# Kernel optimization log

Hardware: AMD Instinct MI355X
Metric: run time of the kernel (lower is better)

Reference implementation:

```python
import jax, jax.numpy as jnp
import numpy as np

D_MODEL = 1024
N_HEADS = 16
D_K = D_MODEL // N_HEADS
SCALE = float(np.sqrt(D_K))


def setup_inputs() -> dict:
    key = jax.random.key(0)
    ks = jax.random.split(key, 11)
    B, L, D = 2, 2048, D_MODEL
    s = 1.0 / np.sqrt(D)
    inp = {
        "q": jax.random.normal(ks[0], (B, L, D), dtype=jnp.float32),
        "k": jax.random.normal(ks[1], (B, L, D), dtype=jnp.float32),
        "v": jax.random.normal(ks[2], (B, L, D), dtype=jnp.float32),
        "Wq": jax.random.normal(ks[3], (D, D), dtype=jnp.float32) * s,
        "bq": jnp.zeros((D,), dtype=jnp.float32),
        "Wk": jax.random.normal(ks[4], (D, D), dtype=jnp.float32) * s,
        "bk": jnp.zeros((D,), dtype=jnp.float32),
        "Wv": jax.random.normal(ks[5], (D, D), dtype=jnp.float32) * s,
        "bv": jnp.zeros((D,), dtype=jnp.float32),
        "Wo": jax.random.normal(ks[6], (D, D), dtype=jnp.float32) * s,
        "bo": jnp.zeros((D,), dtype=jnp.float32),
    }
    return inp


def reference(q, k, v, Wq, bq, Wk, bk, Wv, bv, Wo, bo):
    B, L, D = q.shape
    H, Dk = N_HEADS, D_K
    # projections: [B,L,D] -> [B,H,L,Dk]
    def proj(x, W, b):
        y = x @ W + b
        return y.reshape(B, -1, H, Dk).transpose(0, 2, 1, 3)
    qh = proj(q, Wq, bq)
    kh = proj(k, Wk, bk)
    vh = proj(v, Wv, bv)
    # scores [B,H,Lq,Lk]
    scores = jnp.einsum("bhqd,bhkd->bhqk", qh, kh) / SCALE
    attn = jax.nn.softmax(scores, axis=-1)  # dropout=0.0 -> identity
    out = jnp.einsum("bhqk,bhkd->bhqd", attn, vh)
    out = out.transpose(0, 2, 1, 3).reshape(B, -1, D)
    return out @ Wo + bo
```

## Files before the change

kernel.cpp:

```cpp
#include <hip/hip_runtime.h>
#include <hip/hip_bf16.h>
#include <stdint.h>
#include <stddef.h>

typedef unsigned short ushortT;
typedef __attribute__((ext_vector_type(8))) short bf16x8s;
typedef __attribute__((ext_vector_type(4))) float f32x4;


__device__ __forceinline__ short f2bf(float f) {
  unsigned u = __float_as_uint(f);
  u += 0x7FFFu + ((u >> 16) & 1u);
  return (short)(u >> 16);
}

__device__ __forceinline__ unsigned pk_bf16(float a, float b) {
  __hip_bfloat162 h = __float22bfloat162_rn(make_float2(a, b));
  return *(unsigned*)&h;
}

__device__ __forceinline__ bf16x8s cvt8(const float* src) {
  const float4* p = (const float4*)src;
  float4 a = p[0], b = p[1];
  bf16x8s r;
  r[0] = f2bf(a.x); r[1] = f2bf(a.y); r[2] = f2bf(a.z); r[3] = f2bf(a.w);
  r[4] = f2bf(b.x); r[5] = f2bf(b.y); r[6] = f2bf(b.z); r[7] = f2bf(b.w);
  return r;
}

__device__ __forceinline__ void load_lds16(const ushortT* g, ushortT* l) {
  __builtin_amdgcn_global_load_lds(
      (const __attribute__((address_space(1))) void*)(g),
      (__attribute__((address_space(3))) void*)(l), 16, 0, 0);
}

__global__ __launch_bounds__(256)
void prep(const float* __restrict__ q, const float* __restrict__ k,
          const float* __restrict__ v,
          const float* __restrict__ Wq, const float* __restrict__ Wk,
          const float* __restrict__ Wv, const float* __restrict__ Wo,
          ushortT* __restrict__ Qc, ushortT* __restrict__ Kc,
          ushortT* __restrict__ Vc, ushortT* __restrict__ Wt)
{
  const int z = blockIdx.z;
  if (z < 4) {
    if (blockIdx.x >= 1024) return;
    __shared__ __align__(16) ushortT t[32][33];
    const float* W = (z == 0) ? Wq : (z == 1) ? Wk : (z == 2) ? Wv : Wo;
    ushortT* dst = Wt + (size_t)z * 1024 * 1024;
    const int x = (blockIdx.x & 31) * 32, y = (blockIdx.x >> 5) * 32;
    const int tx = threadIdx.x & 31, ty = threadIdx.x >> 5;
#pragma unroll
    for (int i = ty; i < 32; i += 8)
      t[i][tx] = (ushortT)f2bf(W[(size_t)(y + i) * 1024 + x + tx]);
    __syncthreads();
#pragma unroll
    for (int i = ty; i < 32; i += 8)
      dst[(size_t)(x + i) * 1024 + y + tx] = t[tx][i];
  } else {
    const float* src = (z == 4) ? q : (z == 5) ? k : v;
    ushortT* dst = (z == 4) ? Qc : (z == 5) ? Kc : Vc;
    const size_t i8 = ((size_t)blockIdx.x * 256 + threadIdx.x) * 8;
    *(bf16x8s*)(dst + i8) = cvt8(src + i8);
  }
}

__device__ __forceinline__ void gemm_core_128(
    const ushortT* __restrict__ A, const ushortT* __restrict__ Bt,
    int K, ushortT* As, ushortT* Bs, f32x4 (&acc)[4][4], int m0, int n0)
{
  const int tid  = threadIdx.x;
  const int wave = tid >> 6, lane = tid & 63;
  const int wm = (wave & 1) << 6;
  const int wn = (wave >> 1) << 6;
  const int lr = lane & 15;
  const int lk = (lane >> 4) << 3;

#pragma unroll
  for (int mi = 0; mi < 4; ++mi)
#pragma unroll
    for (int ni = 0; ni < 4; ++ni)
      acc[mi][ni] = (f32x4){0.f, 0.f, 0.f, 0.f};

  for (int k0 = 0; k0 < K; k0 += 32) {
    __syncthreads();
#pragma unroll
    for (int i = 0; i < 2; ++i) {
      const int cc  = tid + (i << 8);
      const int row = cc >> 2;
      const int ko  = (cc & 3) << 3;
      load_lds16(A  + (size_t)(m0 + row) * K + k0 + ko, As + cc * 8);
      load_lds16(Bt + (size_t)(n0 + row) * K + k0 + ko, Bs + cc * 8);
    }
    __syncthreads();

    bf16x8s af[4], bfr[4];
#pragma unroll
    for (int i = 0; i < 4; ++i)
      af[i] = *(const bf16x8s*)(As + (wm + i * 16 + lr) * 32 + lk);
#pragma unroll
    for (int i = 0; i < 4; ++i)
      bfr[i] = *(const bf16x8s*)(Bs + (wn + i * 16 + lr) * 32 + lk);

#pragma unroll
    for (int mi = 0; mi < 4; ++mi)
#pragma unroll
      for (int ni = 0; ni < 4; ++ni)
        acc[mi][ni] = __builtin_amdgcn_mfma_f32_16x16x32_bf16(
            af[mi], bfr[ni], acc[mi][ni], 0, 0, 0);
  }
}

__global__ __launch_bounds__(256)
void proj_gemm(const ushortT* __restrict__ Qc, const ushortT* __restrict__ Kc,
               const ushortT* __restrict__ Vc, const ushortT* __restrict__ WtAll,
               const float* __restrict__ bq, const float* __restrict__ bk,
               const float* __restrict__ bv,
               ushortT* __restrict__ Qh, ushortT* __restrict__ Kh,
               ushortT* __restrict__ Vt)
{
  __shared__ __align__(16) ushortT As[128 * 32];
  __shared__ __align__(16) ushortT Bs[128 * 32];
  const int which = blockIdx.z;
  const ushortT* A  = (which == 0) ? Qc : (which == 1) ? Kc : Vc;
  const ushortT* Bt = WtAll + (size_t)which * 1024 * 1024;
  const float* bias = (which == 0) ? bq : (which == 1) ? bk : bv;
  const int m0 = blockIdx.x * 128, n0 = blockIdx.y * 128;

  f32x4 acc[4][4];
  gemm_core_128(A, Bt, 1024, As, Bs, acc, m0, n0);

  const int lane = threadIdx.x & 63, wave = threadIdx.x >> 6;
  const int wm = (wave & 1) << 6, wn = (wave >> 1) << 6;
  const int lr = lane & 15, quad = lane >> 4;
  const float QSCALE = 0.18033688011112042f;

#pragma unroll
  for (int ni = 0; ni < 4; ++ni) {
    const int n = n0 + wn + ni * 16 + lr;
    const float bias_v = bias[n];
    const int h = n >> 6, d = n & 63;
#pragma unroll
    for (int mi = 0; mi < 4; ++mi) {
#pragma unroll
      for (int r = 0; r < 4; ++r) {
        const int m = m0 + wm + mi * 16 + quad * 4 + r;
        const int b = m >> 11, l = m & 2047;
        float val = acc[mi][ni][r] + bias_v;
        if (which == 0) val *= QSCALE;
        const ushortT o = (ushortT)f2bf(val);
        const size_t bh = (size_t)(b * 16 + h);
        if (which == 0)      Qh[(bh * 2048 + l) * 64 + d] = o;
        else if (which == 1) Kh[(bh * 2048 + l) * 64 + d] = o;
        else                 Vt[(bh * 64 + d) * 2048 + l] = o;
      }
    }
  }
}

__global__ __launch_bounds__(256)
void attn_kernel(const ushortT* __restrict__ Qh, const ushortT* __restrict__ Kh,
                 const ushortT* __restrict__ Vt, ushortT* __restrict__ Ob)
{
  const int b = blockIdx.z, h = blockIdx.y, qt = blockIdx.x;
  const int bh = b * 16 + h;
  const int wave = threadIdx.x >> 6, lane = threadIdx.x & 63;
  const int lr = lane & 15, quad = lane >> 4, lk = quad * 8;
  const int q0 = qt * 64 + wave * 16;

  const ushortT* Q = Qh + ((size_t)bh * 2048 + q0) * 64;
  const ushortT* K = Kh + (size_t)bh * 2048 * 64;
  const ushortT* V = Vt + (size_t)bh * 64 * 2048;

  __shared__ __align__(16) ushortT Ks[64 * 76];
  __shared__ __align__(16) ushortT Vs[64 * 76];
  __shared__ __align__(16) ushortT P4[4][16 * 88];
  ushortT* Pw = P4[wave];

  const bf16x8s qf0 = *(const bf16x8s*)(Q + lr * 64 + lk);
  const bf16x8s qf1 = *(const bf16x8s*)(Q + lr * 64 + 32 + lk);

  f32x4 o[4];
#pragma unroll
  for (int nt = 0; nt < 4; ++nt) o[nt] = (f32x4){0.f, 0.f, 0.f, 0.f};
  float lsum = 0.f;

  const int tid = threadIdx.x;
  const int srow = tid >> 3;
  const int sc8  = (tid & 7) << 3;

  for (int kt = 0; kt < 2048; kt += 64) {
    bf16x8s kch[2], vch[2];
#pragma unroll
    for (int i = 0; i < 2; ++i) {
      const int row = srow + i * 32;
      kch[i] = *(const bf16x8s*)(K + (size_t)(kt + row) * 64 + sc8);
      vch[i] = *(const bf16x8s*)(V + (size_t)row * 2048 + kt + sc8);
    }
    __syncthreads();
#pragma unroll
    for (int i = 0; i < 2; ++i) {
      const int row = srow + i * 32;
      *(bf16x8s*)(Ks + row * 76 + sc8) = kch[i];
      *(bf16x8s*)(Vs + row * 76 + sc8) = vch[i];
    }
    __syncthreads();

    f32x4 s[4];
#pragma unroll
    for (int t = 0; t < 4; ++t) s[t] = (f32x4){0.f, 0.f, 0.f, 0.f};
#pragma unroll
    for (int t = 0; t < 4; ++t) {
      const bf16x8s kf0 = *(const bf16x8s*)(Ks + (t * 16 + lr) * 76 + lk);
      const bf16x8s kf1 = *(const bf16x8s*)(Ks + (t * 16 + lr) * 76 + 32 + lk);
      s[t] = __builtin_amdgcn_mfma_f32_16x16x32_bf16(kf0, qf0, s[t], 0, 0, 0);
      s[t] = __builtin_amdgcn_mfma_f32_16x16x32_bf16(kf1, qf1, s[t], 0, 0, 0);
    }

#pragma unroll
    for (int t = 0; t < 4; ++t) {
      const float e0 = __builtin_amdgcn_exp2f(s[t][0]);
      const float e1 = __builtin_amdgcn_exp2f(s[t][1]);
      const float e2 = __builtin_amdgcn_exp2f(s[t][2]);
      const float e3 = __builtin_amdgcn_exp2f(s[t][3]);
      lsum += (e0 + e1) + (e2 + e3);
      uint2 d;
      d.x = pk_bf16(e0, e1);
      d.y = pk_bf16(e2, e3);
      *(uint2*)(Pw + lr * 88 + t * 16 + quad * 4) = d;
    }
    asm volatile("s_waitcnt lgkmcnt(0)" ::: "memory");

    const bf16x8s pf0 = *(const bf16x8s*)(Pw + lr * 88 + lk);
    const bf16x8s pf1 = *(const bf16x8s*)(Pw + lr * 88 + 32 + lk);
#pragma unroll
    for (int nt = 0; nt < 4; ++nt) {
      const bf16x8s vf0 = *(const bf16x8s*)(Vs + (nt * 16 + lr) * 76 + lk);
      const bf16x8s vf1 = *(const bf16x8s*)(Vs + (nt * 16 + lr) * 76 + 32 + lk);
      o[nt] = __builtin_amdgcn_mfma_f32_16x16x32_bf16(pf0, vf0, o[nt], 0, 0, 0);
      o[nt] = __builtin_amdgcn_mfma_f32_16x16x32_bf16(pf1, vf1, o[nt], 0, 0, 0);
    }
  }

  float* fP = (float*)Pw;
  {
    float s = lsum;
    s += __shfl_xor(s, 16);
    s += __shfl_xor(s, 32);
    fP[lr] = 1.0f / s;
  }
  asm volatile("s_waitcnt lgkmcnt(0)" ::: "memory");
  float invr[4];
#pragma unroll
  for (int r = 0; r < 4; ++r) invr[r] = fP[quad * 4 + r];

#pragma unroll
  for (int nt = 0; nt < 4; ++nt) {
    const int dcol = h * 64 + nt * 16 + lr;
#pragma unroll
    for (int r = 0; r < 4; ++r) {
      const int l = q0 + quad * 4 + r;
      Ob[((size_t)b * 2048 + l) * 1024 + dcol] = (ushortT)f2bf(o[nt][r] * invr[r]);
    }
  }
}

__global__ __launch_bounds__(256)
void out_gemm(const ushortT* __restrict__ Ob, const ushortT* __restrict__ Wto,
              const float* __restrict__ bo, float* __restrict__ C)
{
  __shared__ __align__(16) ushortT As[128 * 32];
  __shared__ __align__(16) ushortT Bs[128 * 32];
  const int m0 = blockIdx.x * 128, n0 = blockIdx.y * 128;

  f32x4 acc[4][4];
  gemm_core_128(Ob, Wto, 1024, As, Bs, acc, m0, n0);

  const int lane = threadIdx.x & 63, wave = threadIdx.x >> 6;
  const int wm = (wave & 1) << 6, wn = (wave >> 1) << 6;
  const int lr = lane & 15, quad = lane >> 4;

#pragma unroll
  for (int ni = 0; ni < 4; ++ni) {
    const int n = n0 + wn + ni * 16 + lr;
    const float bias_v = bo[n];
#pragma unroll
    for (int mi = 0; mi < 4; ++mi) {
#pragma unroll
      for (int r = 0; r < 4; ++r) {
        const int m = m0 + wm + mi * 16 + quad * 4 + r;
        C[(size_t)m * 1024 + n] = acc[mi][ni][r] + bias_v;
      }
    }
  }
}

extern "C" void kernel_launch(void* const* d_in, const int* in_sizes, int n_in,
                              void* d_out, int out_size, void* d_ws, size_t ws_size,
                              hipStream_t stream) {
  const float* q  = (const float*)d_in[0];
  const float* k  = (const float*)d_in[1];
  const float* v  = (const float*)d_in[2];
  const float* Wq = (const float*)d_in[3];
  const float* bq = (const float*)d_in[4];
  const float* Wk = (const float*)d_in[5];
  const float* bk = (const float*)d_in[6];
  const float* Wv = (const float*)d_in[7];
  const float* bv = (const float*)d_in[8];
  const float* Wo = (const float*)d_in[9];
  const float* bo = (const float*)d_in[10];

  char* ws = (char*)d_ws;
  ushortT* Wt = (ushortT*)(ws);
  ushortT* Qh = (ushortT*)(ws + (size_t)(8  << 20));
  ushortT* Kh = (ushortT*)(ws + (size_t)(16 << 20));
  ushortT* Vt = (ushortT*)(ws + (size_t)(24 << 20));
  ushortT* Qc = (ushortT*)(ws + (size_t)(32 << 20));
  ushortT* Kc = (ushortT*)(ws + (size_t)(40 << 20));
  ushortT* Vc = (ushortT*)(ws + (size_t)(48 << 20));
  ushortT* Ob = Qc;

  prep<<<dim3(2048, 1, 7), 256, 0, stream>>>(q, k, v, Wq, Wk, Wv, Wo,
                                             Qc, Kc, Vc, Wt);
  proj_gemm<<<dim3(32, 8, 3), 256, 0, stream>>>(Qc, Kc, Vc, Wt, bq, bk, bv,
                                                Qh, Kh, Vt);
  attn_kernel<<<dim3(32, 16, 2), 256, 0, stream>>>(Qh, Kh, Vt, Ob);
  out_gemm<<<dim3(32, 8), 256, 0, stream>>>(Ob, Wt + (size_t)3 * 1024 * 1024,
                                            bo, (float*)d_out);
}
```

Before: 243.2 us.

## Vectorize weight transpose, deepen GEMM K-step to 64, narrow out_gemm tiles

The weight transpose in prep now does float4 loads and ushort4 stores through a padded LDS tile instead of scalar accesses. The shared GEMM core moves from a K step of 32 to 64, which halves the number of barrier pairs per tile at the cost of twice the LDS. out_gemm switches to 128x64 tiles, doubling the grid to 512 blocks so more CUs have work. The 64-wide LDS rows with a 128-byte stride may cause bank conflicts on the fragment reads.

```diff
diff --git a/kernel.cpp b/kernel.cpp
--- a/kernel.cpp
+++ b/kernel.cpp
@@ -45,18 +45,27 @@
   const int z = blockIdx.z;
   if (z < 4) {
     if (blockIdx.x >= 1024) return;
-    __shared__ __align__(16) ushortT t[32][33];
+    __shared__ __align__(16) ushortT t[32][36];
     const float* W = (z == 0) ? Wq : (z == 1) ? Wk : (z == 2) ? Wv : Wo;
     ushortT* dst = Wt + (size_t)z * 1024 * 1024;
     const int x = (blockIdx.x & 31) * 32, y = (blockIdx.x >> 5) * 32;
-    const int tx = threadIdx.x & 31, ty = threadIdx.x >> 5;
-#pragma unroll
-    for (int i = ty; i < 32; i += 8)
-      t[i][tx] = (ushortT)f2bf(W[(size_t)(y + i) * 1024 + x + tx]);
-    __syncthreads();
-#pragma unroll
-    for (int i = ty; i < 32; i += 8)
-      dst[(size_t)(x + i) * 1024 + y + tx] = t[tx][i];
+    const int tx8 = threadIdx.x & 7, ty = threadIdx.x >> 3;
+    {
+      const float4 f = *(const float4*)(W + (size_t)(y + ty) * 1024 + x + tx8 * 4);
+      ushort4 u;
+      u.x = (ushortT)f2bf(f.x); u.y = (ushortT)f2bf(f.y);
+      u.z = (ushortT)f2bf(f.z); u.w = (ushortT)f2bf(f.w);
+      *(ushort4*)&t[ty][tx8 * 4] = u;
+    }
+    __syncthreads();
+    {
+      ushort4 u;
+      u.x = t[tx8 * 4 + 0][ty];
+      u.y = t[tx8 * 4 + 1][ty];
+      u.z = t[tx8 * 4 + 2][ty];
+      u.w = t[tx8 * 4 + 3][ty];
+      *(ushort4*)(dst + (size_t)(x + ty) * 1024 + y + tx8 * 4) = u;
+    }
   } else {
     const float* src = (z == 4) ? q : (z == 5) ? k : v;
     ushortT* dst = (z == 4) ? Qc : (z == 5) ? Kc : Vc;
@@ -65,9 +74,9 @@
   }
 }
 
-__device__ __forceinline__ void gemm_core_128(
+__device__ __forceinline__ void gemm_core_128_bk64(
     const ushortT* __restrict__ A, const ushortT* __restrict__ Bt,
-    int K, ushortT* As, ushortT* Bs, f32x4 (&acc)[4][4], int m0, int n0)
+    ushortT* As, ushortT* Bs, f32x4 (&acc)[4][4], int m0, int n0)
 {
   const int tid  = threadIdx.x;
   const int wave = tid >> 6, lane = tid & 63;
@@ -82,32 +91,36 @@
     for (int ni = 0; ni < 4; ++ni)
       acc[mi][ni] = (f32x4){0.f, 0.f, 0.f, 0.f};
 
-  for (int k0 = 0; k0 < K; k0 += 32) {
-    __syncthreads();
-#pragma unroll
-    for (int i = 0; i < 2; ++i) {
+  for (int k0 = 0; k0 < 1024; k0 += 64) {
+    __syncthreads();
+#pragma unroll
+    for (int i = 0; i < 4; ++i) {
       const int cc  = tid + (i << 8);
-      const int row = cc >> 2;
-      const int ko  = (cc & 3) << 3;
-      load_lds16(A  + (size_t)(m0 + row) * K + k0 + ko, As + cc * 8);
-      load_lds16(Bt + (size_t)(n0 + row) * K + k0 + ko, Bs + cc * 8);
-    }
-    __syncthreads();
-
-    bf16x8s af[4], bfr[4];
-#pragma unroll
-    for (int i = 0; i < 4; ++i)
-      af[i] = *(const bf16x8s*)(As + (wm + i * 16 + lr) * 32 + lk);
-#pragma unroll
-    for (int i = 0; i < 4; ++i)
-      bfr[i] = *(const bf16x8s*)(Bs + (wn + i * 16 + lr) * 32 + lk);
+      const int row = cc >> 3;
+      const int ko  = (cc & 7) << 3;
+      load_lds16(A  + (size_t)(m0 + row) * 1024 + k0 + ko, As + cc * 8);
+      load_lds16(Bt + (size_t)(n0 + row) * 1024 + k0 + ko, Bs + cc * 8);
+    }
+    __syncthreads();
+
+    bf16x8s af[4][2], bfr[4][2];
+#pragma unroll
+    for (int i = 0; i < 4; ++i) {
+      af[i][0]  = *(const bf16x8s*)(As + (wm + i * 16 + lr) * 64 + lk);
+      af[i][1]  = *(const bf16x8s*)(As + (wm + i * 16 + lr) * 64 + 32 + lk);
+      bfr[i][0] = *(const bf16x8s*)(Bs + (wn + i * 16 + lr) * 64 + lk);
+      bfr[i][1] = *(const bf16x8s*)(Bs + (wn + i * 16 + lr) * 64 + 32 + lk);
+    }
 
 #pragma unroll
     for (int mi = 0; mi < 4; ++mi)
 #pragma unroll
-      for (int ni = 0; ni < 4; ++ni)
+      for (int ni = 0; ni < 4; ++ni) {
         acc[mi][ni] = __builtin_amdgcn_mfma_f32_16x16x32_bf16(
-            af[mi], bfr[ni], acc[mi][ni], 0, 0, 0);
+            af[mi][0], bfr[ni][0], acc[mi][ni], 0, 0, 0);
+        acc[mi][ni] = __builtin_amdgcn_mfma_f32_16x16x32_bf16(
+            af[mi][1], bfr[ni][1], acc[mi][ni], 0, 0, 0);
+      }
   }
 }
 
@@ -119,8 +132,8 @@
                ushortT* __restrict__ Qh, ushortT* __restrict__ Kh,
                ushortT* __restrict__ Vt)
 {
-  __shared__ __align__(16) ushortT As[128 * 32];
-  __shared__ __align__(16) ushortT Bs[128 * 32];
+  __shared__ __align__(16) ushortT As[128 * 64];
+  __shared__ __align__(16) ushortT Bs[128 * 64];
   const int which = blockIdx.z;
   const ushortT* A  = (which == 0) ? Qc : (which == 1) ? Kc : Vc;
   const ushortT* Bt = WtAll + (size_t)which * 1024 * 1024;
@@ -128,7 +141,7 @@
   const int m0 = blockIdx.x * 128, n0 = blockIdx.y * 128;
 
   f32x4 acc[4][4];
-  gemm_core_128(A, Bt, 1024, As, Bs, acc, m0, n0);
+  gemm_core_128_bk64(A, Bt, As, Bs, acc, m0, n0);
 
   const int lane = threadIdx.x & 63, wave = threadIdx.x >> 6;
   const int wm = (wave & 1) << 6, wn = (wave >> 1) << 6;
@@ -269,19 +282,68 @@
 void out_gemm(const ushortT* __restrict__ Ob, const ushortT* __restrict__ Wto,
               const float* __restrict__ bo, float* __restrict__ C)
 {
-  __shared__ __align__(16) ushortT As[128 * 32];
-  __shared__ __align__(16) ushortT Bs[128 * 32];
-  const int m0 = blockIdx.x * 128, n0 = blockIdx.y * 128;
-
-  f32x4 acc[4][4];
-  gemm_core_128(Ob, Wto, 1024, As, Bs, acc, m0, n0);
-
-  const int lane = threadIdx.x & 63, wave = threadIdx.x >> 6;
-  const int wm = (wave & 1) << 6, wn = (wave >> 1) << 6;
-  const int lr = lane & 15, quad = lane >> 4;
-
-#pragma unroll
-  for (int ni = 0; ni < 4; ++ni) {
+  __shared__ __align__(16) ushortT As[128 * 64];
+  __shared__ __align__(16) ushortT Bs[64 * 64];
+  const int m0 = blockIdx.x * 128, n0 = blockIdx.y * 64;
+
+  const int tid  = threadIdx.x;
+  const int wave = tid >> 6, lane = tid & 63;
+  const int wm = (wave & 1) << 6;
+  const int wn = (wave >> 1) << 5;
+  const int lr = lane & 15;
+  const int lk = (lane >> 4) << 3;
+
+  f32x4 acc[4][2];
+#pragma unroll
+  for (int mi = 0; mi < 4; ++mi)
+#pragma unroll
+    for (int ni = 0; ni < 2; ++ni)
+      acc[mi][ni] = (f32x4){0.f, 0.f, 0.f, 0.f};
+
+  for (int k0 = 0; k0 < 1024; k0 += 64) {
+    __syncthreads();
+#pragma unroll
+    for (int i = 0; i < 4; ++i) {
+      const int cc  = tid + (i << 8);
+      const int row = cc >> 3;
+      const int ko  = (cc & 7) << 3;
+      load_lds16(Ob + (size_t)(m0 + row) * 1024 + k0 + ko, As + cc * 8);
+    }
+#pragma unroll
+    for (int i = 0; i < 2; ++i) {
+      const int cc  = tid + (i << 8);
+      const int row = cc >> 3;
+      const int ko  = (cc & 7) << 3;
+      load_lds16(Wto + (size_t)(n0 + row) * 1024 + k0 + ko, Bs + cc * 8);
+    }
+    __syncthreads();
+
+    bf16x8s af[4][2], bfr[2][2];
+#pragma unroll
+    for (int i = 0; i < 4; ++i) {
+      af[i][0] = *(const bf16x8s*)(As + (wm + i * 16 + lr) * 64 + lk);
+      af[i][1] = *(const bf16x8s*)(As + (wm + i * 16 + lr) * 64 + 32 + lk);
+    }
+#pragma unroll
+    for (int i = 0; i < 2; ++i) {
+      bfr[i][0] = *(const bf16x8s*)(Bs + (wn + i * 16 + lr) * 64 + lk);
+      bfr[i][1] = *(const bf16x8s*)(Bs + (wn + i * 16 + lr) * 64 + 32 + lk);
+    }
+
+#pragma unroll
+    for (int mi = 0; mi < 4; ++mi)
+#pragma unroll
+      for (int ni = 0; ni < 2; ++ni) {
+        acc[mi][ni] = __builtin_amdgcn_mfma_f32_16x16x32_bf16(
+            af[mi][0], bfr[ni][0], acc[mi][ni], 0, 0, 0);
+        acc[mi][ni] = __builtin_amdgcn_mfma_f32_16x16x32_bf16(
+            af[mi][1], bfr[ni][1], acc[mi][ni], 0, 0, 0);
+      }
+  }
+
+  const int quad = lane >> 4;
+#pragma unroll
+  for (int ni = 0; ni < 2; ++ni) {
     const int n = n0 + wn + ni * 16 + lr;
     const float bias_v = bo[n];
 #pragma unroll
@@ -325,6 +387,6 @@
   proj_gemm<<<dim3(32, 8, 3), 256, 0, stream>>>(Qc, Kc, Vc, Wt, bq, bk, bv,
                                                 Qh, Kh, Vt);
   attn_kernel<<<dim3(32, 16, 2), 256, 0, stream>>>(Qh, Kh, Vt, Ob);
-  out_gemm<<<dim3(32, 8), 256, 0, stream>>>(Ob, Wt + (size_t)3 * 1024 * 1024,
-                                            bo, (float*)d_out);
-}
+  out_gemm<<<dim3(32, 16), 256, 0, stream>>>(Ob, Wt + (size_t)3 * 1024 * 1024,
+                                             bo, (float*)d_out);
+}
```

Measured after the change: 257.2 us. 5.8% more time.
